# Kernel optimization log

Hardware: AMD Instinct MI355X
Metric: run time of the kernel (lower is better)

The kernel has to match this reference:

```python
import jax, jax.numpy as jnp
import numpy as np

D, L, W, K = 16, 1000000, 64, 8
PAD = (W - 1) // 2  # 31, matches padding1 in the torch code


def setup_inputs() -> dict:
    key = jax.random.key(0)
    kx, kp = jax.random.split(key)
    x = jax.random.normal(kx, (D, L), dtype=jnp.float32)
    # torch uses torch.rand (uniform [0,1)) for each of the K (D,W) parameters
    P = jax.random.uniform(kp, (K, D, W), dtype=jnp.float32)
    return {"x": x, "P": P}


def _fullscan(x, P):
    # x: (D, L); P: (K, D, W)
    p = PAD
    # --- middle positions k in [p, L-W+p]: standard valid correlation ---
    # mid[k_out, o] = sum_{d,m} x[d, o+m] * P[k_out, d, m], position k = o + p
    mid = jax.lax.conv_general_dilated(
        x[None],                      # (1, D, L)
        P,                            # (K, D, W)
        window_strides=(1,),
        padding="VALID",
        dimension_numbers=("NCH", "OIH", "NCH"),
    )[0]                              # (K, L-W+1)
    # --- left edge k in [0, p): data x[:, :k+W-p] * kernel[:, :k+W-p] ---
    # prefix[i, m] = sum_d x[d, m] * P[i, d, m] over the first W samples
    tl = jnp.einsum("dm,kdm->km", x[:, :W], P)        # (K, W)
    left_c = jnp.cumsum(tl, axis=1)                    # prefix sums
    left = left_c[:, W - p - 1 : W - 1]                # (K, p)
    # --- right edge k in (L-W+p, L): data x[:, k-p:] * kernel[:, W+k-L-p:] ---
    tr = jnp.einsum("dm,kdm->km", x[:, L - W :], P)    # (K, W)
    suf = jnp.cumsum(tr[:, ::-1], axis=1)[:, ::-1]     # suffix sums: suf[:, t] = sum_{m>=t}
    right = suf[:, 1 : W - p]                          # (K, W-1-p)
    y = jnp.concatenate([left, mid, right], axis=1)    # (K, L)
    return y.reshape(-1, 1)                            # (K*L, 1)


def reference(x, P):
    return _fullscan(x, P)
```

## Files before the change

### kernel.cpp

```cpp
#include <hip/hip_runtime.h>


constexpr int D    = 16;
constexpr int L    = 1000000;
constexpr int W    = 64;
constexpr int K    = 8;
constexpr int PADL = 31;
constexpr int NMID = L - W + 1;
constexpr int TPB  = 256;
constexpr int OTW  = 8;
constexpr int CTW  = OTW + 2;
constexpr int BLK_OUT = 4 * OTW * 32;
constexpr int XS   = 1104;
constexpr int NBLK = (NMID + BLK_OUT - 1) / BLK_OUT;
constexpr int NGRID = NBLK + K;

typedef __attribute__((ext_vector_type(8)))  short short8;
typedef __attribute__((ext_vector_type(16))) float floatx16;

__device__ __forceinline__ unsigned short f2bf(float f) {
    union { float f; unsigned u; } v; v.f = f;
    unsigned u = v.u + 0x7fff + ((v.u >> 16) & 1);
    return (unsigned short)(u >> 16);
}

__global__ __launch_bounds__(TPB, 3) void fullscan_mid(
    const float* __restrict__ x, const float* __restrict__ P,
    const unsigned short* __restrict__ afr, float* __restrict__ out)
{
    __shared__ __align__(16) unsigned short xs[XS * 16];
    const int bid = blockIdx.x;
    const int tid = threadIdx.x;

    if (bid >= NBLK) {
        const int k = bid - NBLK;
        const int j = tid;
        if (j < PADL) {
            float acc = 0.0f;
            for (int m = 0; m <= 32 + j; ++m)
#pragma unroll
                for (int d = 0; d < D; ++d)
                    acc = fmaf(x[d * L + m], P[(k * D + d) * W + m], acc);
            out[k * L + j] = acc;
        } else if (j < 2 * PADL + 1) {
            const int jj = j - PADL;
            float acc = 0.0f;
            for (int m = jj + 1; m < W; ++m)
#pragma unroll
                for (int d = 0; d < D; ++d)
                    acc = fmaf(x[d * L + (L - W) + m], P[(k * D + d) * W + m], acc);
            out[k * L + PADL + NMID + jj] = acc;
        }
        return;
    }

    const int s0   = bid * BLK_OUT;
    const int lane = tid & 63;
    const int wv   = tid >> 6;

    short8 A[16];
#pragma unroll
    for (int c = 0; c < 16; ++c)
        A[c] = *(const short8*)(afr + (c * 64 + lane) * 8);

    {
        const int pl = tid & 63;
        const int dq = tid >> 6;
        const float* xr0 = x + (4 * dq + 0) * L + s0;
        const float* xr1 = x + (4 * dq + 1) * L + s0;
        const float* xr2 = x + (4 * dq + 2) * L + s0;
        const float* xr3 = x + (4 * dq + 3) * L + s0;
#pragma unroll 1
        for (int b = 0; b < XS; b += 64) {
            const int pos = b + pl;
            if (pos < XS) {
                const bool ok = (s0 + pos) < L;
                const float v0 = ok ? xr0[pos] : 0.0f;
                const float v1 = ok ? xr1[pos] : 0.0f;
                const float v2 = ok ? xr2[pos] : 0.0f;
                const float v3 = ok ? xr3[pos] : 0.0f;
                unsigned long long w =
                    (unsigned long long)f2bf(v0)
                  | ((unsigned long long)f2bf(v1) << 16)
                  | ((unsigned long long)f2bf(v2) << 32)
                  | ((unsigned long long)f2bf(v3) << 48);
                const int swz = (pos >> 2) & 1;
                *(unsigned long long*)&xs[pos * 16 + ((dq * 4) ^ (swz * 8))] = w;
            }
        }
    }
    __syncthreads();

    const int n  = lane & 31;
    const int h  = lane >> 5;
    const int hb = h * 8;
    const int wbase = wv * OTW;

    floatx16 accW[3];

#pragma unroll
    for (int jj = 0; jj < CTW; ++jj) {
        floatx16 acc;
#pragma unroll
        for (int r = 0; r < 16; ++r) acc[r] = 0.0f;
        const int p0 = (wbase + jj) * 32 + n;

        short8 Bc = *(const short8*)
            &xs[p0 * 16 + (hb ^ (((p0 >> 2) & 1) * 8))];
#pragma unroll
        for (int c = 0; c < 16; ++c) {
            short8 Bn = Bc;
            if (c < 15) {
                const int pos = p0 + c + 1;
                Bn = *(const short8*)
                    &xs[pos * 16 + (hb ^ (((pos >> 2) & 1) * 8))];
            }
            acc = __builtin_amdgcn_mfma_f32_32x32x16_bf16(A[c], Bc, acc, 0, 0, 0);
            Bc = Bn;
        }
        accW[jj % 3] = acc;

        if (jj >= 2) {
            const int ot = jj - 2;
            const floatx16 a0 = accW[(jj - 2) % 3];
            const floatx16 a1 = accW[(jj - 1) % 3];
            const floatx16 a2 = accW[jj % 3];
            const int t = s0 + (wbase + ot) * 32 + n;
#pragma unroll
            for (int kk = 0; kk < 4; ++kk) {
                const float g1t = (n >= 16) ? a0[kk + 4]  : a1[kk + 4];
                const float g3t = (n >= 16) ? a1[kk + 12] : a2[kk + 12];
                const float v = a0[kk] + a1[kk + 8]
                              + __shfl_xor(g1t, 16, 64)
                              + __shfl_xor(g3t, 16, 64);
                if (t < NMID)
                    out[(kk + 4 * h) * L + PADL + t] = v;
            }
        }
    }
}

__global__ void fullscan_prep(const float* __restrict__ P,
                              unsigned short* __restrict__ afr)
{
    const int u = blockIdx.x * 256 + threadIdx.x;
    const int c = u >> 9, lane = (u >> 3) & 63, j = u & 7;
    const int m = lane & 31, h = lane >> 5;
    const int k = m & 7, g = m >> 3;
    const int d = 8 * h + j;
    const int w = 16 * g + c;
    afr[u] = f2bf(P[(k * D + d) * W + w]);
}

extern "C" void kernel_launch(void* const* d_in, const int* in_sizes, int n_in,
                              void* d_out, int out_size, void* d_ws, size_t ws_size,
                              hipStream_t stream)
{
    const float* x = (const float*)d_in[0];
    const float* P = (const float*)d_in[1];
    float* out = (float*)d_out;
    unsigned short* afr = (unsigned short*)d_ws;

    hipLaunchKernelGGL(fullscan_prep, dim3(32), dim3(256), 0, stream, P, afr);
    hipLaunchKernelGGL(fullscan_mid, dim3(NGRID), dim3(TPB), 0, stream,
                       x, P, afr, out);
}
```

Before: 138.5 us.

## Halve per-wave output tiles, compress accumulator carry state, deepen LDS prefetch

Cuts the output tiles per wave from 8 to 4, which shrinks the LDS staging buffer, and raises the launch-bounds occupancy hint from 3 to 4 blocks per CU. The three full 16-float accumulators kept across tiles are replaced by a few 4-float partial sums that are combined step by step, which lowers register pressure. The LDS B-fragment prefetch goes from one ahead to a three-deep ring, and the global staging loop is unrolled by 2. In exchange there are more blocks, so the two halo tiles per wave are a larger share of the MFMA work and the A fragments are reloaded more often.

```diff
diff --git a/kernel.cpp b/kernel.cpp
--- a/kernel.cpp
+++ b/kernel.cpp
@@ -8,10 +8,10 @@
 constexpr int PADL = 31;
 constexpr int NMID = L - W + 1;
 constexpr int TPB  = 256;
-constexpr int OTW  = 8;
+constexpr int OTW  = 4;
 constexpr int CTW  = OTW + 2;
 constexpr int BLK_OUT = 4 * OTW * 32;
-constexpr int XS   = 1104;
+constexpr int XS   = 592;
 constexpr int NBLK = (NMID + BLK_OUT - 1) / BLK_OUT;
 constexpr int NGRID = NBLK + K;
 
@@ -24,7 +24,7 @@
     return (unsigned short)(u >> 16);
 }
 
-__global__ __launch_bounds__(TPB, 3) void fullscan_mid(
+__global__ __launch_bounds__(TPB, 4) void fullscan_mid(
     const float* __restrict__ x, const float* __restrict__ P,
     const unsigned short* __restrict__ afr, float* __restrict__ out)
 {
@@ -70,7 +70,7 @@
         const float* xr1 = x + (4 * dq + 1) * L + s0;
         const float* xr2 = x + (4 * dq + 2) * L + s0;
         const float* xr3 = x + (4 * dq + 3) * L + s0;
-#pragma unroll 1
+#pragma unroll 2
         for (int b = 0; b < XS; b += 64) {
             const int pos = b + pl;
             if (pos < XS) {
@@ -96,7 +96,7 @@
     const int hb = h * 8;
     const int wbase = wv * OTW;
 
-    floatx16 accW[3];
+    float pendA[4], pendB[4], prev4[4], prev12[4];
 
 #pragma unroll
     for (int jj = 0; jj < CTW; ++jj) {
@@ -105,37 +105,46 @@
         for (int r = 0; r < 16; ++r) acc[r] = 0.0f;
         const int p0 = (wbase + jj) * 32 + n;
 
-        short8 Bc = *(const short8*)
-            &xs[p0 * 16 + (hb ^ (((p0 >> 2) & 1) * 8))];
+        short8 Bf[3];
+#pragma unroll
+        for (int c = 0; c < 3; ++c) {
+            const int pos = p0 + c;
+            Bf[c] = *(const short8*)
+                &xs[pos * 16 + (hb ^ (((pos >> 2) & 1) * 8))];
+        }
 #pragma unroll
         for (int c = 0; c < 16; ++c) {
-            short8 Bn = Bc;
-            if (c < 15) {
-                const int pos = p0 + c + 1;
-                Bn = *(const short8*)
+            acc = __builtin_amdgcn_mfma_f32_32x32x16_bf16(A[c], Bf[c % 3], acc, 0, 0, 0);
+            if (c + 3 < 16) {
+                const int pos = p0 + c + 3;
+                Bf[c % 3] = *(const short8*)
                     &xs[pos * 16 + (hb ^ (((pos >> 2) & 1) * 8))];
             }
-            acc = __builtin_amdgcn_mfma_f32_32x32x16_bf16(A[c], Bc, acc, 0, 0, 0);
-            Bc = Bn;
         }
-        accW[jj % 3] = acc;
 
         if (jj >= 2) {
             const int ot = jj - 2;
-            const floatx16 a0 = accW[(jj - 2) % 3];
-            const floatx16 a1 = accW[(jj - 1) % 3];
-            const floatx16 a2 = accW[jj % 3];
             const int t = s0 + (wbase + ot) * 32 + n;
 #pragma unroll
             for (int kk = 0; kk < 4; ++kk) {
-                const float g1t = (n >= 16) ? a0[kk + 4]  : a1[kk + 4];
-                const float g3t = (n >= 16) ? a1[kk + 12] : a2[kk + 12];
-                const float v = a0[kk] + a1[kk + 8]
-                              + __shfl_xor(g1t, 16, 64)
-                              + __shfl_xor(g3t, 16, 64);
+                const float g3t = (n >= 16) ? prev12[kk] : acc[kk + 12];
+                const float v = pendA[kk] + __shfl_xor(g3t, 16, 64);
                 if (t < NMID)
                     out[(kk + 4 * h) * L + PADL + t] = v;
             }
+        }
+        if (jj >= 1) {
+#pragma unroll
+            for (int kk = 0; kk < 4; ++kk) {
+                const float g1t = (n >= 16) ? prev4[kk] : acc[kk + 4];
+                pendA[kk] = pendB[kk] + acc[kk + 8] + __shfl_xor(g1t, 16, 64);
+            }
+        }
+#pragma unroll
+        for (int kk = 0; kk < 4; ++kk) {
+            pendB[kk]  = acc[kk];
+            prev4[kk]  = acc[kk + 4];
+            prev12[kk] = acc[kk + 12];
         }
     }
 }
```

After: 151.0 us. 9.0% more time.
